# Kernel optimization log

Measured on AMD Instinct MI355X. Metric: run time of the kernel, lower is better.

Reference implementation:

```python
import jax, jax.numpy as jnp
import numpy as np

K = 3          # kernel size (hardcoded in module)
PAD = 1        # kernel_size // 2
K2 = K * K


def conv3x3(x, w, b):
    """Standard 3x3 stride-1 same-padding conv, NCHW / OIHW."""
    y = jax.lax.conv_general_dilated(
        x, w, window_strides=(1, 1), padding=[(PAD, PAD), (PAD, PAD)],
        dimension_numbers=('NCHW', 'OIHW', 'NCHW'))
    return y + b[None, :, None, None]


def setup_inputs() -> dict:
    key = jax.random.key(0)
    ks = jax.random.split(key, 8)
    B, C, O, H, W = 8, 64, 64, 128, 128
    x = jax.random.normal(ks[0], (B, C, H, W), dtype=jnp.float32)
    # offset conv: 2*K2 output channels; small init so offsets stay modest
    w_off = jax.random.normal(ks[1], (2 * K2, C, K, K), dtype=jnp.float32) * 0.05
    b_off = jnp.zeros((2 * K2,), dtype=jnp.float32)
    # modulator conv: K2 output channels
    w_mod = jax.random.normal(ks[2], (K2, C, K, K), dtype=jnp.float32) * 0.05
    b_mod = jnp.zeros((K2,), dtype=jnp.float32)
    # main deformable conv weight/bias
    w = jax.random.normal(ks[3], (O, C, K, K), dtype=jnp.float32) * (1.0 / np.sqrt(C * K2))
    b = jax.random.normal(ks[4], (O,), dtype=jnp.float32) * 0.01
    return {"x": x, "w_off": w_off, "b_off": b_off,
            "w_mod": w_mod, "b_mod": b_mod, "w": w, "b": b}


def reference(x, w_off, b_off, w_mod, b_mod, w, b):
    B, C, H, W = x.shape
    O = w.shape[0]

    # offset / modulator heads (torchvision layout: channel 2k = dy, 2k+1 = dx)
    offset = conv3x3(x, w_off, b_off)                       # [B, 2*K2, H, W]
    mask = 2.0 * jax.nn.sigmoid(conv3x3(x, w_mod, b_mod))   # [B, K2, H, W]
    off = offset.reshape(B, K2, 2, H, W)
    dy, dx = off[:, :, 0], off[:, :, 1]                     # [B, K2, H, W]

    # base sampling grid: p = (h - pad + ki, w - pad + kj) + learned offset
    ki = (jnp.arange(K2) // K).astype(x.dtype)
    kj = (jnp.arange(K2) % K).astype(x.dtype)
    hh = jnp.arange(H, dtype=x.dtype)
    ww = jnp.arange(W, dtype=x.dtype)
    py = dy + hh[None, None, :, None] - PAD + ki[None, :, None, None]
    px = dx + ww[None, None, None, :] - PAD + kj[None, :, None, None]

    def sample_one(x_b, py_b, px_b):
        # x_b: [C, H, W]; py_b, px_b: [K2, H, W]. Bilinear, zero outside.
        y0 = jnp.floor(py_b)
        x0 = jnp.floor(px_b)
        wy = py_b - y0                                      # [K2, H, W]
        wx = px_b - x0
        y0i = y0.astype(jnp.int32)
        x0i = x0.astype(jnp.int32)

        def gather(yi, xi):
            valid = (yi >= 0) & (yi < H) & (xi >= 0) & (xi < W)
            v = x_b[:, jnp.clip(yi, 0, H - 1), jnp.clip(xi, 0, W - 1)]  # [C,K2,H,W]
            return v * valid[None].astype(x_b.dtype)

        v00 = gather(y0i, x0i)
        v01 = gather(y0i, x0i + 1)
        v10 = gather(y0i + 1, x0i)
        v11 = gather(y0i + 1, x0i + 1)
        return (v00 * (1 - wy) * (1 - wx) + v01 * (1 - wy) * wx
                + v10 * wy * (1 - wx) + v11 * wy * wx)       # [C, K2, H, W]

    sampled = jax.vmap(sample_one)(x, py, px)               # [B, C, K2, H, W]

    # modulated contraction over (c, k): GEMM-like core
    wk = w.reshape(O, C, K2)
    out = jnp.einsum('bckhw,bkhw,ock->bohw', sampled, mask, wk)
    return out + b[None, :, None, None]
```

## Files before the change

### kernel.cpp

```cpp
#include <hip/hip_runtime.h>
#include <math.h>

#define H_ 128
#define W_ 128
#define C_ 64
#define O_ 64
#define B_ 8
#define K2_ 9
#define HWSZ (H_*W_)

typedef float f2u __attribute__((ext_vector_type(2), aligned(4)));

__global__ __launch_bounds__(256) void prep_weights_k(
    const float* __restrict__ w, const float* __restrict__ w_off,
    const float* __restrict__ w_mod, float* __restrict__ wt,
    float* __restrict__ wom) {
    int id = blockIdx.x * 256 + threadIdx.x;
    if (id < K2_ * C_ * O_) {
        int o = id & (O_ - 1);
        int c = (id >> 6) & (C_ - 1);
        int k = id / (C_ * O_);
        wt[id] = w[(o * C_ + c) * K2_ + k];
    }
    int id2 = id - K2_ * C_ * O_;
    if (id2 >= 0 && id2 < C_ * 243) {
        int k = id2 % 9;
        int tt = (id2 / 9) % 27;
        int c = id2 / 243;
        float v = (tt < 18) ? w_off[(tt * C_ + c) * K2_ + k]
                            : w_mod[((tt - 18) * C_ + c) * K2_ + k];
        wom[id2] = v;
    }
}

__global__ __launch_bounds__(512, 4) void deform_fused_k(
    const float* __restrict__ x,
    const float* __restrict__ wom, const float* __restrict__ b_off,
    const float* __restrict__ b_mod, const float* __restrict__ wt,
    const float* __restrict__ bias, float* __restrict__ out) {
    __shared__ float red[O_ * 256];

    int b     = blockIdx.x & 7;
    int strip = blockIdx.x >> 3;
    int tid   = threadIdx.x;
    int t     = tid & 255;
    int half  = tid >> 8;
    int c0    = __builtin_amdgcn_readfirstlane(half << 5);
    int p     = strip * 256 + t;
    int w     = p & (W_ - 1);
    int h     = p >> 7;

    const float* xb = x + (b * C_ + c0) * HWSZ;

    {
        int offs[9];
        float valid[9];
#pragma unroll
        for (int i = 0; i < 9; i++) {
            int dy = i / 3 - 1, dx = i % 3 - 1;
            int yy = h + dy, xx = w + dx;
            bool v = (yy >= 0 && yy < H_ && xx >= 0 && xx < W_);
            int yc = min(max(yy, 0), H_ - 1);
            int xc = min(max(xx, 0), W_ - 1);
            offs[i] = yc * W_ + xc;
            valid[i] = v ? 1.0f : 0.0f;
        }

        float acc27[27];
#pragma unroll
        for (int o = 0; o < 27; o++) acc27[o] = 0.0f;

        float v[9];
#pragma unroll
        for (int i = 0; i < 9; i++) v[i] = xb[offs[i]] * valid[i];

        for (int c = 0; c < 32; c++) {
            const float* xn = xb + min(c + 1, 31) * HWSZ;
            float vn[9];
#pragma unroll
            for (int i = 0; i < 9; i++) vn[i] = xn[offs[i]] * valid[i];

            const float* wc = wom + (c0 + c) * 243;
#pragma unroll
            for (int o = 0; o < 27; o++) {
#pragma unroll
                for (int kk = 0; kk < 9; kk++) acc27[o] += v[kk] * wc[o * 9 + kk];
            }
#pragma unroll
            for (int i = 0; i < 9; i++) v[i] = vn[i];
        }

        if (half) {
#pragma unroll
            for (int o = 0; o < 27; o++) red[o * 256 + t] = acc27[o];
        }
        __syncthreads();
        if (!half) {
#pragma unroll
            for (int k = 0; k < 9; k++) {
                float dy = acc27[2 * k]     + red[(2 * k)     * 256 + t] + b_off[2 * k];
                float dx = acc27[2 * k + 1] + red[(2 * k + 1) * 256 + t] + b_off[2 * k + 1];
                float mm = acc27[18 + k]    + red[(18 + k)    * 256 + t] + b_mod[k];
                float mask = 2.0f / (1.0f + __expf(-mm));
                float py = dy + (float)h - 1.0f + (float)(k / 3);
                float px = dx + (float)w - 1.0f + (float)(k % 3);
                red[(27 + 3 * k + 0) * 256 + t] = py;
                red[(27 + 3 * k + 1) * 256 + t] = px;
                red[(27 + 3 * k + 2) * 256 + t] = mask;
            }
        }
        __syncthreads();
    }

    float acc[O_];
#pragma unroll
    for (int o = 0; o < O_; o++) acc[o] = 0.0f;

    for (int k = 0; k < 9; k++) {
        float py = red[(27 + 3 * k + 0) * 256 + t];
        float px = red[(27 + 3 * k + 1) * 256 + t];
        float m  = red[(27 + 3 * k + 2) * 256 + t];

        float y0f = floorf(py), x0f = floorf(px);
        float wy = py - y0f, wx = px - x0f;
        int y0 = (int)y0f, x0 = (int)x0f;
        int y1 = y0 + 1;
        float vy0 = (y0 >= 0 && y0 < H_) ? 1.0f : 0.0f;
        float vy1 = (y1 >= 0 && y1 < H_) ? 1.0f : 0.0f;
        float vx0 = (x0 >= 0 && x0 < W_) ? 1.0f : 0.0f;
        float vx1 = (x0 >= -1 && x0 < W_ - 1) ? 1.0f : 0.0f;
        int y0c = min(max(y0, 0), H_ - 1), y1c = min(max(y1, 0), H_ - 1);

        float w00 = (1.0f - wy) * (1.0f - wx) * vy0 * vx0 * m;
        float w01 = (1.0f - wy) * wx * vy0 * vx1 * m;
        float w10 = wy * (1.0f - wx) * vy1 * vx0 * m;
        float w11 = wy * wx * vy1 * vx1 * m;

        int lc   = min(max(x0, 0), W_ - 2);
        bool xlo = (x0 < 0);
        bool xhi = (x0 > W_ - 2);
        float a00 = xhi ? 0.0f : (xlo ? w01 : w00);
        float a01 = xlo ? 0.0f : (xhi ? w00 : w01);
        float a10 = xhi ? 0.0f : (xlo ? w11 : w10);
        float a11 = xlo ? 0.0f : (xhi ? w10 : w11);

        int r0 = y0c * W_ + lc;
        int r1 = y1c * W_ + lc;

        const float* wp = wt + k * (C_ * O_) + c0 * O_;
        for (int c = 0; c < 32; c++) {
            const float* xc = xb + c * HWSZ;
            f2u f0 = *(const f2u*)(xc + r0);
            f2u f1 = *(const f2u*)(xc + r1);
            float s = a00 * f0.x + a01 * f0.y + a10 * f1.x + a11 * f1.y;
            const float* wpc = wp + c * O_;
#pragma unroll
            for (int o = 0; o < O_; o++) acc[o] += s * wpc[o];
        }
    }

    __syncthreads();
    if (half) {
#pragma unroll
        for (int o = 0; o < O_; o++) red[o * 256 + t] = acc[o];
    }
    __syncthreads();
    if (!half) {
        int obase = b * O_ * HWSZ + p;
#pragma unroll
        for (int o = 0; o < O_; o++)
            out[obase + o * HWSZ] = acc[o] + red[o * 256 + t] + bias[o];
    }
}

extern "C" void kernel_launch(void* const* d_in, const int* in_sizes, int n_in,
                              void* d_out, int out_size, void* d_ws, size_t ws_size,
                              hipStream_t stream) {
    const float* x     = (const float*)d_in[0];
    const float* w_off = (const float*)d_in[1];
    const float* b_off = (const float*)d_in[2];
    const float* w_mod = (const float*)d_in[3];
    const float* b_mod = (const float*)d_in[4];
    const float* w     = (const float*)d_in[5];
    const float* bias  = (const float*)d_in[6];
    float* out = (float*)d_out;

    float* wt  = (float*)d_ws;
    float* wom = wt + K2_ * C_ * O_;

    const int nPrep = K2_ * C_ * O_ + C_ * 243;
    hipLaunchKernelGGL(prep_weights_k, dim3((nPrep + 255) / 256), dim3(256),
                       0, stream, w, w_off, w_mod, wt, wom);
    hipLaunchKernelGGL(deform_fused_k, dim3(512), dim3(512), 0, stream,
                       x, wom, b_off, b_mod, wt, bias, out);
}
```

Measured before the change: 350.7 us.

## Stage 16-row input window in LDS and split output channels across half-blocks

The fused deformable conv now stages a 16-row window of two interleaved channels into double-buffered LDS, and both the offset/modulator conv and the bilinear sampling read from it, falling back to global loads when a sample lands outside the window. Work is split by output channel (27→28 padded, 14 per half for the offset conv, 32 per half for the main GEMM) instead of by input channel, which removes the cross-half reductions and halves the accumulator register count. The cost is more barriers per channel pair, sampled values passed through LDS, and a divergent slow path for large offsets.

```diff
diff --git a/kernel.cpp b/kernel.cpp
--- a/kernel.cpp
+++ b/kernel.cpp
@@ -8,6 +8,9 @@
 #define B_ 8
 #define K2_ 9
 #define HWSZ (H_*W_)
+#define WIN_ 16
+#define AOUT_ 8192
+#define SBUF_ 8192
 
 typedef float f2u __attribute__((ext_vector_type(2), aligned(4)));
 
@@ -23,12 +26,13 @@
         wt[id] = w[(o * C_ + c) * K2_ + k];
     }
     int id2 = id - K2_ * C_ * O_;
-    if (id2 >= 0 && id2 < C_ * 243) {
+    if (id2 >= 0 && id2 < C_ * 252) {
         int k = id2 % 9;
-        int tt = (id2 / 9) % 27;
-        int c = id2 / 243;
-        float v = (tt < 18) ? w_off[(tt * C_ + c) * K2_ + k]
-                            : w_mod[((tt - 18) * C_ + c) * K2_ + k];
+        int tt = (id2 / 9) % 28;
+        int c = id2 / 252;
+        float v = 0.0f;
+        if (tt < 18)      v = w_off[(tt * C_ + c) * K2_ + k];
+        else if (tt < 27) v = w_mod[((tt - 18) * C_ + c) * K2_ + k];
         wom[id2] = v;
     }
 }
@@ -38,88 +42,102 @@
     const float* __restrict__ wom, const float* __restrict__ b_off,
     const float* __restrict__ b_mod, const float* __restrict__ wt,
     const float* __restrict__ bias, float* __restrict__ out) {
-    __shared__ float red[O_ * 256];
+    __shared__ float lds[15360];
 
     int b     = blockIdx.x & 7;
     int strip = blockIdx.x >> 3;
     int tid   = threadIdx.x;
     int t     = tid & 255;
     int half  = tid >> 8;
-    int c0    = __builtin_amdgcn_readfirstlane(half << 5);
     int p     = strip * 256 + t;
     int w     = p & (W_ - 1);
     int h     = p >> 7;
-
-    const float* xb = x + (b * C_ + c0) * HWSZ;
-
-    {
-        int offs[9];
-        float valid[9];
+    int h0    = strip * 2;
+    int lo    = min(max(h0 - 7, 0), H_ - WIN_);
+
+    const float* xB = x + b * C_ * HWSZ;
+
+    int srow  = tid >> 5;
+    int scol  = (tid & 31) * 4;
+    int sgoff = (lo + srow) * W_ + scol;
+
+#define STAGE(CHPAIR, BUF)                                                     \
+    {                                                                          \
+        const float* s0 = xB + (2 * (CHPAIR)) * HWSZ + sgoff;                  \
+        float4 ga = *(const float4*)s0;                                        \
+        float4 gb = *(const float4*)(s0 + HWSZ);                               \
+        float2* d = (float2*)lds + (BUF) * 2048 + srow * W_ + scol;            \
+        d[0] = make_float2(ga.x, gb.x); d[1] = make_float2(ga.y, gb.y);        \
+        d[2] = make_float2(ga.z, gb.z); d[3] = make_float2(ga.w, gb.w);        \
+    }
+
+    int aoff[9]; float avalid[9];
+#pragma unroll
+    for (int i = 0; i < 9; i++) {
+        int dy = i / 3 - 1, dx = i % 3 - 1;
+        int yy = h + dy, xx = w + dx;
+        bool v = (yy >= 0 && yy < H_ && xx >= 0 && xx < W_);
+        int yc = min(max(yy, 0), H_ - 1);
+        int xc = min(max(xx, 0), W_ - 1);
+        aoff[i] = (yc - lo) * W_ + xc;
+        avalid[i] = v ? 1.0f : 0.0f;
+    }
+
+    float accA[14];
+#pragma unroll
+    for (int o = 0; o < 14; o++) accA[o] = 0.0f;
+    int o0A9 = half * 14 * 9;
+
+    STAGE(0, 0);
+    __syncthreads();
+
+    for (int cp = 0; cp < 32; cp++) {
+        float4 ga, gb;
+        if (cp < 31) {
+            const float* sn = xB + (2 * (cp + 1)) * HWSZ + sgoff;
+            ga = *(const float4*)sn;
+            gb = *(const float4*)(sn + HWSZ);
+        }
+        const float2* S = (const float2*)lds + (cp & 1) * 2048;
+        float vA[9], vB[9];
 #pragma unroll
         for (int i = 0; i < 9; i++) {
-            int dy = i / 3 - 1, dx = i % 3 - 1;
-            int yy = h + dy, xx = w + dx;
-            bool v = (yy >= 0 && yy < H_ && xx >= 0 && xx < W_);
-            int yc = min(max(yy, 0), H_ - 1);
-            int xc = min(max(xx, 0), W_ - 1);
-            offs[i] = yc * W_ + xc;
-            valid[i] = v ? 1.0f : 0.0f;
-        }
-
-        float acc27[27];
-#pragma unroll
-        for (int o = 0; o < 27; o++) acc27[o] = 0.0f;
-
-        float v[9];
-#pragma unroll
-        for (int i = 0; i < 9; i++) v[i] = xb[offs[i]] * valid[i];
-
-        for (int c = 0; c < 32; c++) {
-            const float* xn = xb + min(c + 1, 31) * HWSZ;
-            float vn[9];
-#pragma unroll
-            for (int i = 0; i < 9; i++) vn[i] = xn[offs[i]] * valid[i];
-
-            const float* wc = wom + (c0 + c) * 243;
-#pragma unroll
-            for (int o = 0; o < 27; o++) {
-#pragma unroll
-                for (int kk = 0; kk < 9; kk++) acc27[o] += v[kk] * wc[o * 9 + kk];
-            }
-#pragma unroll
-            for (int i = 0; i < 9; i++) v[i] = vn[i];
-        }
-
-        if (half) {
-#pragma unroll
-            for (int o = 0; o < 27; o++) red[o * 256 + t] = acc27[o];
+            float2 tv = S[aoff[i]];
+            vA[i] = tv.x * avalid[i];
+            vB[i] = tv.y * avalid[i];
+        }
+        const float* wA = wom + (2 * cp) * 252 + o0A9;
+        const float* wB = wA + 252;
+#pragma unroll
+        for (int o = 0; o < 14; o++) {
+#pragma unroll
+            for (int i = 0; i < 9; i++)
+                accA[o] += vA[i] * wA[o * 9 + i] + vB[i] * wB[o * 9 + i];
+        }
+        if (cp < 31) {
+            float2* d = (float2*)lds + ((cp + 1) & 1) * 2048 + srow * W_ + scol;
+            d[0] = make_float2(ga.x, gb.x); d[1] = make_float2(ga.y, gb.y);
+            d[2] = make_float2(ga.z, gb.z); d[3] = make_float2(ga.w, gb.w);
         }
         __syncthreads();
-        if (!half) {
-#pragma unroll
-            for (int k = 0; k < 9; k++) {
-                float dy = acc27[2 * k]     + red[(2 * k)     * 256 + t] + b_off[2 * k];
-                float dx = acc27[2 * k + 1] + red[(2 * k + 1) * 256 + t] + b_off[2 * k + 1];
-                float mm = acc27[18 + k]    + red[(18 + k)    * 256 + t] + b_mod[k];
-                float mask = 2.0f / (1.0f + __expf(-mm));
-                float py = dy + (float)h - 1.0f + (float)(k / 3);
-                float px = dx + (float)w - 1.0f + (float)(k % 3);
-                red[(27 + 3 * k + 0) * 256 + t] = py;
-                red[(27 + 3 * k + 1) * 256 + t] = px;
-                red[(27 + 3 * k + 2) * 256 + t] = mask;
-            }
-        }
-        __syncthreads();
-    }
-
-    float acc[O_];
-#pragma unroll
-    for (int o = 0; o < O_; o++) acc[o] = 0.0f;
-
-    for (int k = 0; k < 9; k++) {
-        float py = red[(27 + 3 * k + 0) * 256 + t];
-        float px = red[(27 + 3 * k + 1) * 256 + t];
-        float m  = red[(27 + 3 * k + 2) * 256 + t];
+    }
+
+#pragma unroll
+    for (int o = 0; o < 14; o++) lds[AOUT_ + (half * 14 + o) * 256 + t] = accA[o];
+    __syncthreads();
+
+    float ca0[5], ca1[5], ca2[5], ca3[5];
+    int   cpk[5];
+    int   kbase = half ? 5 : 0;
+#pragma unroll
+    for (int i = 0; i < 5; i++) {
+        int k = (i < 4) ? (kbase + i) : 4;
+        float dy = lds[AOUT_ + (2 * k) * 256 + t]     + b_off[2 * k];
+        float dx = lds[AOUT_ + (2 * k + 1) * 256 + t] + b_off[2 * k + 1];
+        float mm = lds[AOUT_ + (18 + k) * 256 + t]    + b_mod[k];
+        float mask = 2.0f / (1.0f + __expf(-mm));
+        float py = dy + (float)h - 1.0f + (float)(k / 3);
+        float px = dx + (float)w - 1.0f + (float)(k % 3);
 
         float y0f = floorf(py), x0f = floorf(px);
         float wy = py - y0f, wx = px - x0f;
@@ -131,46 +149,99 @@
         float vx1 = (x0 >= -1 && x0 < W_ - 1) ? 1.0f : 0.0f;
         int y0c = min(max(y0, 0), H_ - 1), y1c = min(max(y1, 0), H_ - 1);
 
-        float w00 = (1.0f - wy) * (1.0f - wx) * vy0 * vx0 * m;
-        float w01 = (1.0f - wy) * wx * vy0 * vx1 * m;
-        float w10 = wy * (1.0f - wx) * vy1 * vx0 * m;
-        float w11 = wy * wx * vy1 * vx1 * m;
+        float w00 = (1.0f - wy) * (1.0f - wx) * vy0 * vx0 * mask;
+        float w01 = (1.0f - wy) * wx * vy0 * vx1 * mask;
+        float w10 = wy * (1.0f - wx) * vy1 * vx0 * mask;
+        float w11 = wy * wx * vy1 * vx1 * mask;
 
         int lc   = min(max(x0, 0), W_ - 2);
         bool xlo = (x0 < 0);
         bool xhi = (x0 > W_ - 2);
-        float a00 = xhi ? 0.0f : (xlo ? w01 : w00);
-        float a01 = xlo ? 0.0f : (xhi ? w00 : w01);
-        float a10 = xhi ? 0.0f : (xlo ? w11 : w10);
-        float a11 = xlo ? 0.0f : (xhi ? w10 : w11);
-
-        int r0 = y0c * W_ + lc;
-        int r1 = y1c * W_ + lc;
-
-        const float* wp = wt + k * (C_ * O_) + c0 * O_;
-        for (int c = 0; c < 32; c++) {
-            const float* xc = xb + c * HWSZ;
-            f2u f0 = *(const f2u*)(xc + r0);
-            f2u f1 = *(const f2u*)(xc + r1);
-            float s = a00 * f0.x + a01 * f0.y + a10 * f1.x + a11 * f1.y;
-            const float* wpc = wp + c * O_;
-#pragma unroll
-            for (int o = 0; o < O_; o++) acc[o] += s * wpc[o];
-        }
-    }
-
-    __syncthreads();
-    if (half) {
-#pragma unroll
-        for (int o = 0; o < O_; o++) red[o * 256 + t] = acc[o];
-    }
-    __syncthreads();
-    if (!half) {
-        int obase = b * O_ * HWSZ + p;
-#pragma unroll
-        for (int o = 0; o < O_; o++)
-            out[obase + o * HWSZ] = acc[o] + red[o * 256 + t] + bias[o];
-    }
+        ca0[i] = xhi ? 0.0f : (xlo ? w01 : w00);
+        ca1[i] = xlo ? 0.0f : (xhi ? w00 : w01);
+        ca2[i] = xhi ? 0.0f : (xlo ? w11 : w10);
+        ca3[i] = xlo ? 0.0f : (xhi ? w10 : w11);
+
+        int r0c = min(max(y0c - lo, 0), WIN_ - 1);
+        int r1c = min(max(y1c - lo, 0), WIN_ - 1);
+        int in0 = (y0c >= lo && y0c < lo + WIN_) ? 1 : 0;
+        int in1 = (y1c >= lo && y1c < lo + WIN_) ? 1 : 0;
+        cpk[i] = lc | (r0c << 7) | (r1c << 11) | (in0 << 15) | (in1 << 16)
+               | (y0c << 17) | (y1c << 24);
+    }
+    __syncthreads();
+
+    float acc[32];
+#pragma unroll
+    for (int o = 0; o < 32; o++) acc[o] = 0.0f;
+    int o0 = half << 5;
+    float2* sb = (float2*)(lds + SBUF_);
+
+    STAGE(0, 0);
+    __syncthreads();
+
+    for (int cp = 0; cp < 32; cp++) {
+        float4 ga, gb;
+        if (cp < 31) {
+            const float* sn = xB + (2 * (cp + 1)) * HWSZ + sgoff;
+            ga = *(const float4*)sn;
+            gb = *(const float4*)(sn + HWSZ);
+        }
+        const float2* S   = (const float2*)lds + (cp & 1) * 2048;
+        const float* xc2  = xB + 2 * cp * HWSZ;
+
+#pragma unroll
+        for (int i = 0; i < 5; i++) {
+            if (i == 4 && half) break;
+            int pk = cpk[i];
+            int lc = pk & 127;
+            int i0 = ((pk >> 7) & 15) * W_ + lc;
+            int i1 = ((pk >> 11) & 15) * W_ + lc;
+            float2 p00 = S[i0], p01 = S[i0 + 1];
+            float2 p10 = S[i1], p11 = S[i1 + 1];
+            if (__builtin_expect((pk & (1 << 15)) == 0, 0)) {
+                const float* xa = xc2 + ((pk >> 17) & 127) * W_ + lc;
+                f2u g0 = *(const f2u*)xa;
+                f2u g1 = *(const f2u*)(xa + HWSZ);
+                p00 = make_float2(g0.x, g1.x);
+                p01 = make_float2(g0.y, g1.y);
+            }
+            if (__builtin_expect((pk & (1 << 16)) == 0, 0)) {
+                const float* xa = xc2 + ((pk >> 24) & 127) * W_ + lc;
+                f2u g0 = *(const f2u*)xa;
+                f2u g1 = *(const f2u*)(xa + HWSZ);
+                p10 = make_float2(g0.x, g1.x);
+                p11 = make_float2(g0.y, g1.y);
+            }
+            float sA = ca0[i] * p00.x + ca1[i] * p01.x + ca2[i] * p10.x + ca3[i] * p11.x;
+            float sB = ca0[i] * p00.y + ca1[i] * p01.y + ca2[i] * p10.y + ca3[i] * p11.y;
+            int k = (i < 4) ? (kbase + i) : 4;
+            sb[k * 256 + t] = make_float2(sA, sB);
+        }
+        if (cp < 31) {
+            float2* d = (float2*)lds + ((cp + 1) & 1) * 2048 + srow * W_ + scol;
+            d[0] = make_float2(ga.x, gb.x); d[1] = make_float2(ga.y, gb.y);
+            d[2] = make_float2(ga.z, gb.z); d[3] = make_float2(ga.w, gb.w);
+        }
+        __syncthreads();
+
+        const float* wk = wt + (2 * cp) * O_ + o0;
+#pragma unroll
+        for (int k = 0; k < 9; k++) {
+            float2 s = sb[k * 256 + t];
+            const float* wA = wk + k * (C_ * O_);
+            const float* wB = wA + O_;
+#pragma unroll
+            for (int o = 0; o < 32; o++) acc[o] += s.x * wA[o] + s.y * wB[o];
+        }
+        __syncthreads();
+    }
+#undef STAGE
+
+    int obase = b * O_ * HWSZ + o0 * HWSZ + p;
+#pragma unroll
+    for (int o = 0; o < 32; o++)
+        out[obase + o * HWSZ] = acc[o] + bias[o0 + o];
 }
 
 extern "C" void kernel_launch(void* const* d_in, const int* in_sizes, int n_in,
@@ -188,7 +259,7 @@
     float* wt  = (float*)d_ws;
     float* wom = wt + K2_ * C_ * O_;
 
-    const int nPrep = K2_ * C_ * O_ + C_ * 243;
+    const int nPrep = K2_ * C_ * O_ + C_ * 252;
     hipLaunchKernelGGL(prep_weights_k, dim3((nPrep + 255) / 256), dim3(256),
                        0, stream, w, w_off, w_mod, wt, wom);
     hipLaunchKernelGGL(deform_fused_k, dim3(512), dim3(512), 0, stream,
```

Result: slower. 1.366 ms (+289.3%).
